# Optimization experiments

Measured on AMD Instinct MI355X. Metric: run time of the kernel, lower is better.

Reference implementation:

```python
import jax, jax.numpy as jnp
import numpy as np
from jax.scipy.linalg import cho_solve

N = 4096        # num nodes
D = 256         # in_dim == out_dim
NUM_HOPS = 2
R = 32          # subspace_dim
ETA = 0.5
EPS_SUB = 0.5   # eps in coeff = r / (n * eps^2)
LN_EPS = 1e-5


def setup_inputs() -> dict:
    rng = np.random.default_rng(0)
    K = NUM_HOPS + 1
    # sparse-ish binary adjacency mask with self loops
    mask = (rng.random((N, N)) < 0.002).astype(np.float32)
    mask = np.maximum(mask, np.eye(N, dtype=np.float32))
    deg = mask.sum(axis=1, keepdims=True)
    A = (mask / deg).astype(np.float32)          # row-stochastic propagation
    L = (np.eye(N, dtype=np.float32) - A)        # normalized Laplacian
    H = rng.standard_normal((N, D)).astype(np.float32)
    # orthonormal subspace bases per hop, as in __init__ (QR of randn)
    U = np.stack([np.linalg.qr(rng.standard_normal((D, R)))[0][:, :R] for _ in range(K)]).astype(np.float32)
    lambda_laps = np.full((K,), 0.1, dtype=np.float32)
    hop_weights = np.full((K,), 1.0 / K, dtype=np.float32)
    threshold = np.full((D,), 0.05, dtype=np.float32)
    gamma = np.ones((D,), dtype=np.float32)
    beta = np.zeros((D,), dtype=np.float32)
    return {
        "H": jnp.asarray(H), "A": jnp.asarray(A), "adj_mask": jnp.asarray(mask),
        "L": jnp.asarray(L), "U": jnp.asarray(U),
        "lambda_laps": jnp.asarray(lambda_laps), "hop_weights": jnp.asarray(hop_weights),
        "threshold": jnp.asarray(threshold), "gamma": jnp.asarray(gamma), "beta": jnp.asarray(beta),
    }


def reference(H, A, adj_mask, L, U, lambda_laps, hop_weights, threshold, gamma, beta):
    n, d = H.shape
    r = U.shape[-1]
    # multi-hop propagation
    hops = [H]
    Hk = H
    for _ in range(NUM_HOPS):
        Hk = A @ Hk
        hops.append(Hk)
    w = jax.nn.softmax(hop_weights)
    laps = jax.nn.softplus(lambda_laps)
    coeff = r / (n * EPS_SUB ** 2)
    neg = (1.0 - adj_mask) * -1e9
    I_r = jnp.eye(r, dtype=H.dtype)
    agg = jnp.zeros_like(H)        # accumulates grad_k.T, shape [n, d]
    lap_total = jnp.zeros_like(H)
    for k, H_k in enumerate(hops):
        Uk = U[k]                  # [d, r]
        Zk = Uk.T @ H_k.T          # [r, n]
        M = I_r + coeff * (Zk @ Zk.T)              # [r, r], SPD
        Lc = jnp.linalg.cholesky(M)
        M_inv = cho_solve((Lc, True), I_r)         # cholesky_inverse
        MZ = M_inv @ Zk                            # [r, n]
        scores = Zk.T @ MZ + neg                   # [n, n] masked subspace attention
        alpha = jax.nn.softmax(scores, axis=1)
        grad_k = (Uk @ (MZ @ alpha.T)).T           # [n, d]
        agg = agg + w[k] * grad_k
        lap_total = lap_total + laps[k] * (L @ H_k)
    H_half = H + ETA * agg - ETA * lap_total
    # soft-threshold (proj is None since in_dim == out_dim)
    H_out = jnp.sign(H_half) * jax.nn.relu(jnp.abs(H_half) - threshold[None, :])
    H_out = H_out + H              # residual
    mu = H_out.mean(axis=-1, keepdims=True)
    var = H_out.var(axis=-1, keepdims=True)
    H_out = (H_out - mu) / jnp.sqrt(var + LN_EPS) * gamma + beta
    # orthogonality loss over all (k, l) pairs
    K = U.shape[0]
    orth_loss = jnp.asarray(0.0, dtype=H.dtype)
    for k in range(K):
        for l in range(k, K):
            G = U[k].T @ U[l]
            orth_loss = orth_loss + jnp.sum(((G - I_r) if l == k else G) ** 2)
    lap_smooth = jnp.sum(H_out * (L @ H_out))  # trace(H^T L H)
    return H_out, orth_loss, lap_smooth, jax.lax.stop_gradient(w)
```

## Files before the change

kernel.cpp:

```cpp
#include <hip/hip_runtime.h>
#include <math.h>

#define NN 4096
#define DD 256
#define KK 3
#define RR 32
#define MAXNNZ 128

static constexpr float ETA    = 0.5f;
static constexpr float COEFF  = 0.03125f;
static constexpr float LN_EPSF = 1e-5f;

#define OFF_H1   0
#define OFF_H2   (NN*DD)
#define OFF_H3   (2*NN*DD)
#define OFF_Y    (3*NN*DD)
#define OFF_P    (OFF_Y + KK*NN*RR)
#define OFF_M    (OFF_P + KK*NN*RR)
#define OFF_MINV (OFF_M + KK*RR*RR)
#define OFF_SCAL (OFF_MINV + KK*RR*RR)
#define OFF_NNZ  (OFF_SCAL + 8)
#define OFF_COLS (OFF_NNZ + NN)
#define OFF_VALS (OFF_COLS + NN*MAXNNZ)
#define OFF_PART (OFF_VALS + NN*MAXNNZ)
#define OFF_ORTH (OFF_PART + NN/4)
#define OFF_W    (OFF_ORTH + 8)

__global__ __launch_bounds__(256, 4)
void k_csr_prep(const float* __restrict__ A, int* __restrict__ nnz,
                int* __restrict__ cols, float* __restrict__ vals,
                const float* __restrict__ hw, const float* __restrict__ ll,
                const float* __restrict__ U,
                float* __restrict__ ws, float* __restrict__ out,
                const float* __restrict__ H) {
  int b = blockIdx.x;
  int t = threadIdx.x;
  if (b >= NN/2) {
    int p = b - NN/2;
    if (p == 6) {
      if (t == 0) {
        float m = fmaxf(fmaxf(hw[0], hw[1]), hw[2]);
        float e0 = expf(hw[0]-m), e1 = expf(hw[1]-m), e2 = expf(hw[2]-m);
        float s = e0 + e1 + e2;
        float w0 = e0/s, w1 = e1/s, w2 = e2/s;
        ws[OFF_SCAL+0] = w0; ws[OFF_SCAL+1] = w1; ws[OFF_SCAL+2] = w2;
        for (int k = 0; k < KK; ++k) {
          float x = ll[k];
          ws[OFF_SCAL+3+k] = (x > 20.f) ? x : log1pf(expf(x));
        }
        out[NN*DD + 2] = w0; out[NN*DD + 3] = w1; out[NN*DD + 4] = w2;
      }
      for (int idx = t; idx < KK*RR*RR; idx += 256) {
        int rr2 = idx % (RR*RR);
        ws[OFF_M + idx] = ((rr2 / RR) == (rr2 % RR)) ? 1.f : 0.f;
      }
      return;
    }
    int k = (p < 3) ? 0 : ((p < 5) ? 1 : 2);
    int l = (p < 3) ? p : ((p < 5) ? p - 2 : 2);
    int a0 = t >> 5, bb = t & 31;
    float s0 = 0.f, s1 = 0.f, s2 = 0.f, s3 = 0.f;
    for (int dd = 0; dd < DD; ++dd) {
      float ul = U[(size_t)l*DD*RR + dd*RR + bb];
      const float* uk = U + (size_t)k*DD*RR + dd*RR;
      s0 += uk[a0]      * ul;
      s1 += uk[a0 + 8]  * ul;
      s2 += uk[a0 + 16] * ul;
      s3 += uk[a0 + 24] * ul;
    }
    if (k == l && bb == a0)      s0 -= 1.f;
    if (k == l && bb == a0 + 8)  s1 -= 1.f;
    if (k == l && bb == a0 + 16) s2 -= 1.f;
    if (k == l && bb == a0 + 24) s3 -= 1.f;
    float sq = s0*s0 + s1*s1 + s2*s2 + s3*s3;
    #pragma unroll
    for (int o = 32; o > 0; o >>= 1) sq += __shfl_xor(sq, o, 64);
    __shared__ float red[4];
    if ((t & 63) == 0) red[t >> 6] = sq;
    __syncthreads();
    if (t == 0) ws[OFF_ORTH + p] = red[0] + red[1] + red[2] + red[3];
    return;
  }
  int w = t >> 6, lane = t & 63;
  int r = w >> 1, h2 = w & 1;
  int i = b * 2 + r;
  __shared__ int   cbuf[2][2][MAXNNZ];
  __shared__ float vbuf[2][2][MAXNNZ];
  __shared__ int   csr_c[2][MAXNNZ];
  __shared__ float csr_v[2][MAXNNZ];
  __shared__ int   cnts[4];
  __shared__ int   nnzs[2];
  __shared__ float Hs[2][2][DD];
  __shared__ float Hs2[2][2][2][DD];
  const float4* row4 = (const float4*)(A + (size_t)i * NN);
  float4 vv[8];
  #pragma unroll
  for (int it = 0; it < 8; ++it) vv[it] = row4[h2*512 + it*64 + lane];
  unsigned long long lower = lane ? (~0ull >> (64 - lane)) : 0ull;
  int base = 0;
  #pragma unroll
  for (int it = 0; it < 8; ++it) {
    float4 v = vv[it];
    int jb = (h2*512 + it*64 + lane) * 4;
    unsigned long long mx = __ballot(v.x != 0.f);
    unsigned long long my = __ballot(v.y != 0.f);
    unsigned long long mz = __ballot(v.z != 0.f);
    unsigned long long mw = __ballot(v.w != 0.f);
    int before = __popcll(mx & lower) + __popcll(my & lower)
               + __popcll(mz & lower) + __popcll(mw & lower);
    int p0 = base + before;
    int bx = (mx >> lane) & 1, by = (my >> lane) & 1, bz = (mz >> lane) & 1;
    if (v.x != 0.f && p0 < MAXNNZ)  { cbuf[r][h2][p0] = jb;   vbuf[r][h2][p0] = v.x; }
    int p1 = p0 + bx;
    if (v.y != 0.f && p1 < MAXNNZ)  { cbuf[r][h2][p1] = jb+1; vbuf[r][h2][p1] = v.y; }
    int p2 = p1 + by;
    if (v.z != 0.f && p2 < MAXNNZ)  { cbuf[r][h2][p2] = jb+2; vbuf[r][h2][p2] = v.z; }
    int p3 = p2 + bz;
    if (v.w != 0.f && p3 < MAXNNZ)  { cbuf[r][h2][p3] = jb+3; vbuf[r][h2][p3] = v.w; }
    base += __popcll(mx) + __popcll(my) + __popcll(mz) + __popcll(mw);
  }
  if (lane == 0) cnts[w] = base < MAXNNZ ? base : MAXNNZ;
  __syncthreads();
  {
    int rr = t >> 7, e0 = t & 127;
    int ii = b * 2 + rr;
    int n0 = cnts[rr*2], n1 = cnts[rr*2 + 1];
    int n = n0 + n1; if (n > MAXNNZ) n = MAXNNZ;
    int npad = (n + 7) & ~7;
    for (int e = e0; e < npad; e += 128) {
      int c; float v;
      if (e < n) {
        if (e < n0) { c = cbuf[rr][0][e];      v = vbuf[rr][0][e]; }
        else        { c = cbuf[rr][1][e - n0]; v = vbuf[rr][1][e - n0]; }
      } else { c = ii; v = 0.f; }
      cols[ii*MAXNNZ + e] = c;
      vals[ii*MAXNNZ + e] = v;
      csr_c[rr][e] = c;
      csr_v[rr][e] = v;
    }
    if (e0 == 0) { nnz[ii] = n; nnzs[rr] = n; }
  }
  __syncthreads();
  {
    int rI = w >> 1, hf = w & 1;
    int row = b * 2 + rI;
    int d4 = lane * 4;
    int n2 = nnzs[rI], npad2 = (n2 + 7) & ~7;
    float4 acc = {0.f, 0.f, 0.f, 0.f};
    float4 own = {0.f, 0.f, 0.f, 0.f};
    for (int e0i = hf*8; e0i < npad2; e0i += 16) {
      int4 c0 = *(const int4*)&csr_c[rI][e0i];
      int4 c1 = *(const int4*)&csr_c[rI][e0i + 4];
      float4 v0 = *(const float4*)&csr_v[rI][e0i];
      float4 v1 = *(const float4*)&csr_v[rI][e0i + 4];
      float4 x0 = *(const float4*)(H + (size_t)c0.x*DD + d4);
      float4 x1 = *(const float4*)(H + (size_t)c0.y*DD + d4);
      float4 x2 = *(const float4*)(H + (size_t)c0.z*DD + d4);
      float4 x3 = *(const float4*)(H + (size_t)c0.w*DD + d4);
      float4 x4 = *(const float4*)(H + (size_t)c1.x*DD + d4);
      float4 x5 = *(const float4*)(H + (size_t)c1.y*DD + d4);
      float4 x6 = *(const float4*)(H + (size_t)c1.z*DD + d4);
      float4 x7 = *(const float4*)(H + (size_t)c1.w*DD + d4);
      if (c0.x == row) own = x0;
      if (c0.y == row) own = x1;
      if (c0.z == row) own = x2;
      if (c0.w == row) own = x3;
      if (c1.x == row) own = x4;
      if (c1.y == row) own = x5;
      if (c1.z == row) own = x6;
      if (c1.w == row) own = x7;
      acc.x += v0.x*x0.x + v0.y*x1.x + v0.z*x2.x + v0.w*x3.x + v1.x*x4.x + v1.y*x5.x + v1.z*x6.x + v1.w*x7.x;
      acc.y += v0.x*x0.y + v0.y*x1.y + v0.z*x2.y + v0.w*x3.y + v1.x*x4.y + v1.y*x5.y + v1.z*x6.y + v1.w*x7.y;
      acc.z += v0.x*x0.z + v0.y*x1.z + v0.z*x2.z + v0.w*x3.z + v1.x*x4.z + v1.y*x5.z + v1.z*x6.z + v1.w*x7.z;
      acc.w += v0.x*x0.w + v0.y*x1.w + v0.z*x2.w + v0.w*x3.w + v1.x*x4.w + v1.y*x5.w + v1.z*x6.w + v1.w*x7.w;
    }
    *(float4*)&Hs2[rI][0][hf][d4] = own;
    *(float4*)&Hs2[rI][1][hf][d4] = acc;
  }
  __syncthreads();
  float* H1 = ws + OFF_H1;
  for (int idx = t; idx < 2*2*DD; idx += 256) {
    int rI2 = idx >> 9, j = (idx >> 8) & 1, d = idx & 255;
    float v2 = Hs2[rI2][j][0][d] + Hs2[rI2][j][1][d];
    Hs[rI2][j][d] = v2;
    if (j == 1) H1[(size_t)(b*2 + rI2)*DD + d] = v2;
  }
  __syncthreads();
  {
    int rI = w >> 1;
    int row = b * 2 + rI;
    int useAcc = w & 1;
    const float* Up = U + (size_t)useAcc*DD*RR;
    float* Yp = ws + OFF_Y + (size_t)useAcc*NN*RR;
    int c = lane & 31, h = lane >> 5;
    float part = 0.f;
    #pragma unroll 8
    for (int d = h*128; d < h*128 + 128; ++d) part += Hs[rI][useAcc][d] * Up[d*RR + c];
    part += __shfl_xor(part, 32, 64);
    if (h == 0) Yp[(size_t)row*RR + c] = part;
  }
}

__device__ __forceinline__ void spmv_quad(const float* __restrict__ X, int row, int lane,
                                          const int* __restrict__ nnz,
                                          const int* __restrict__ cols,
                                          const float* __restrict__ vals,
                                          float4& acc, float4& own) {
  int d4 = lane * 4;
  int n = nnz[row];
  int npad = (n + 7) & ~7;
  const int* ci = cols + row*MAXNNZ;
  const float* vi = vals + row*MAXNNZ;
  for (int e0 = 0; e0 < npad; e0 += 8) {
    int4 c0 = *(const int4*)(ci + e0);
    int4 c1 = *(const int4*)(ci + e0 + 4);
    float4 v0 = *(const float4*)(vi + e0);
    float4 v1 = *(const float4*)(vi + e0 + 4);
    float4 x0 = *(const float4*)(X + (size_t)c0.x*DD + d4);
    float4 x1 = *(const float4*)(X + (size_t)c0.y*DD + d4);
    float4 x2 = *(const float4*)(X + (size_t)c0.z*DD + d4);
    float4 x3 = *(const float4*)(X + (size_t)c0.w*DD + d4);
    float4 x4 = *(const float4*)(X + (size_t)c1.x*DD + d4);
    float4 x5 = *(const float4*)(X + (size_t)c1.y*DD + d4);
    float4 x6 = *(const float4*)(X + (size_t)c1.z*DD + d4);
    float4 x7 = *(const float4*)(X + (size_t)c1.w*DD + d4);
    if (c0.x == row) own = x0;
    if (c0.y == row) own = x1;
    if (c0.z == row) own = x2;
    if (c0.w == row) own = x3;
    if (c1.x == row) own = x4;
    if (c1.y == row) own = x5;
    if (c1.z == row) own = x6;
    if (c1.w == row) own = x7;
    acc.x += v0.x*x0.x + v0.y*x1.x + v0.z*x2.x + v0.w*x3.x + v1.x*x4.x + v1.y*x5.x + v1.z*x6.x + v1.w*x7.x;
    acc.y += v0.x*x0.y + v0.y*x1.y + v0.z*x2.y + v0.w*x3.y + v1.x*x4.y + v1.y*x5.y + v1.z*x6.y + v1.w*x7.y;
    acc.z += v0.x*x0.z + v0.y*x1.z + v0.z*x2.z + v0.w*x3.z + v1.x*x4.z + v1.y*x5.z + v1.z*x6.z + v1.w*x7.z;
    acc.w += v0.x*x0.w + v0.y*x1.w + v0.z*x2.w + v0.w*x3.w + v1.x*x4.w + v1.y*x5.w + v1.z*x6.w + v1.w*x7.w;
  }
}

__global__ void k_spmvy(const float* __restrict__ X, float* __restrict__ Hout,
                        const int* __restrict__ nnz, const int* __restrict__ cols,
                        const float* __restrict__ vals,
                        const float* __restrict__ Uo, float* __restrict__ Yo,
                        const float* __restrict__ Un, float* __restrict__ Yn,
                        const float* __restrict__ Yg, float* __restrict__ Mg) {
  int t = threadIdx.x;
  if (blockIdx.x >= NN/4) {
    if (!Yg) return;
    int gb = blockIdx.x - NN/4;
    int k = gb >> 5, g = gb & 31;
    __shared__ float Ys[128*RR];
    const float* Yk = Yg + (size_t)k*NN*RR + (size_t)g*128*RR;
    for (int idx = t; idx < 128*RR; idx += 256) Ys[idx] = Yk[idx];
    __syncthreads();
    int a = t >> 3, b4 = (t & 7) * 4;
    float s0 = 0.f, s1 = 0.f, s2 = 0.f, s3 = 0.f;
    for (int i = 0; i < 128; ++i) {
      float ya = Ys[i*RR + a];
      s0 += ya * Ys[i*RR + b4];
      s1 += ya * Ys[i*RR + b4 + 1];
      s2 += ya * Ys[i*RR + b4 + 2];
      s3 += ya * Ys[i*RR + b4 + 3];
    }
    atomicAdd(&Mg[k*RR*RR + a*RR + b4],     COEFF * s0);
    atomicAdd(&Mg[k*RR*RR + a*RR + b4 + 1], COEFF * s1);
    atomicAdd(&Mg[k*RR*RR + a*RR + b4 + 2], COEFF * s2);
    atomicAdd(&Mg[k*RR*RR + a*RR + b4 + 3], COEFF * s3);
    return;
  }
  int r = t >> 6, lane = t & 63;
  int row = blockIdx.x * 4 + r;
  int d4 = lane * 4;
  float4 acc = {0.f, 0.f, 0.f, 0.f};
  float4 own = {0.f, 0.f, 0.f, 0.f};
  spmv_quad(X, row, lane, nnz, cols, vals, acc, own);
  *(float4*)(Hout + (size_t)row*DD + d4) = acc;
  if (!Uo && !Un) return;
  __shared__ float Hs[4][2][DD];
  *(float4*)&Hs[r][0][d4] = own;
  *(float4*)&Hs[r][1][d4] = acc;
  __syncthreads();
  int c = lane & 31, h = lane >> 5;
  if (Uo) {
    float part = 0.f;
    #pragma unroll 8
    for (int d = h*128; d < h*128 + 128; ++d) part += Hs[r][0][d] * Uo[d*RR + c];
    part += __shfl_xor(part, 32, 64);
    if (h == 0) Yo[(size_t)row*RR + c] = part;
  }
  if (Un) {
    float part = 0.f;
    #pragma unroll 8
    for (int d = h*128; d < h*128 + 128; ++d) part += Hs[r][1][d] * Un[d*RR + c];
    part += __shfl_xor(part, 32, 64);
    if (h == 0) Yn[(size_t)row*RR + c] = part;
  }
}

__global__ __launch_bounds__(1024) void k_gram(const float* __restrict__ Yk, float* __restrict__ Mk) {
  __shared__ float Ys[128*RR];
  int t = threadIdx.x;
  const float* Yb = Yk + (size_t)blockIdx.x*128*RR;
  for (int idx = t; idx < 128*RR; idx += 1024) Ys[idx] = Yb[idx];
  __syncthreads();
  int a = t >> 5, b = t & 31;
  float s = 0.f;
  for (int i = 0; i < 128; ++i) s += Ys[i*RR + a] * Ys[i*RR + b];
  atomicAdd(&Mk[a*RR + b], COEFF * s);
}

__global__ __launch_bounds__(256) void k_gj(const float* __restrict__ M, float* __restrict__ Minv,
                                            const float* __restrict__ U, float* __restrict__ W) {
  int k = blockIdx.x;
  int g = blockIdx.y;
  int t = threadIdx.x;
  __shared__ float B[RR][2*RR + 1];
  for (int idx = t; idx < RR*2*RR; idx += 256) {
    int r = idx >> 6, c = idx & 63;
    B[r][c] = (c < RR) ? M[k*RR*RR + r*RR + c] : ((c - RR == r) ? 1.f : 0.f);
  }
  __syncthreads();
  if (t < 64) {
    for (int p = 0; p < RR; ++p) {
      float rd = 1.f / B[p][p];
      float pb = B[p][t] * rd;
      float f[RR];
      #pragma unroll
      for (int r = 0; r < RR; ++r) f[r] = B[r][p];
      B[p][t] = pb;
      #pragma unroll
      for (int r = 0; r < RR; ++r) {
        if (r == p) continue;
        B[r][t] -= f[r] * pb;
      }
    }
  }
  __syncthreads();
  if (g == 0)
    for (int idx = t; idx < RR*RR; idx += 256)
      Minv[k*RR*RR + idx] = B[idx >> 5][RR + (idx & 31)];
  for (int e = 0; e < 8; ++e) {
    int idx = t + e*256;
    int d = g*64 + (idx >> 5), rr2 = idx & 31;
    const float* ud = U + (size_t)k*DD*RR + (size_t)d*RR;
    float s = 0.f;
    #pragma unroll
    for (int a = 0; a < RR; ++a) s += ud[a] * B[a][RR + rr2];
    W[(size_t)k*DD*RR + (size_t)d*RR + rr2] = s;
  }
}

__global__ __launch_bounds__(256) void k_attn(const float* __restrict__ Y, const float* __restrict__ Minv,
                       float* __restrict__ P, const int* __restrict__ nnz,
                       const int* __restrict__ cols, const float* __restrict__ vals,
                       const float* __restrict__ H2, float* __restrict__ H3) {
  int k = blockIdx.y;
  int t = threadIdx.x;
  int w = t >> 6, lane = t & 63;
  if (blockIdx.x >= NN/4) {
    if (k != 0) return;
    int row = (blockIdx.x - NN/4) * 4 + w;
    float4 acc = {0.f, 0.f, 0.f, 0.f};
    float4 own;
    spmv_quad(H2, row, lane, nnz, cols, vals, acc, own);
    *(float4*)(H3 + (size_t)row*DD + lane*4) = acc;
    return;
  }
  int i = blockIdx.x * 4 + w;
  const float* Yk = Y + (size_t)k*NN*RR;
  __shared__ float Mi[RR*RR];
  __shared__ float Yi[4][RR];
  __shared__ float qv[4][RR];
  __shared__ float sc[4][MAXNNZ];
  __shared__ float Yc[4][32][RR + 1];
  for (int idx = t; idx < RR*RR; idx += 256) Mi[idx] = Minv[k*RR*RR + idx];
  if (lane < RR) Yi[w][lane] = Yk[(size_t)i*RR + lane];
  sc[w][lane] = -1e30f; sc[w][lane+64] = -1e30f;
  __syncthreads();
  if (lane < RR) {
    float s = 0.f;
    #pragma unroll 8
    for (int a = 0; a < RR; ++a) s += Mi[a*RR + lane] * Yi[w][a];
    qv[w][lane] = s;
  }
  int g = lane >> 2, a4 = lane & 3;
  const float* qq = &qv[w][8*a4];
  float q0 = qq[0], q1 = qq[1], q2 = qq[2], q3 = qq[3];
  float q4 = qq[4], q5 = qq[5], q6 = qq[6], q7 = qq[7];
  int n = nnz[i], npad = (n + 7) & ~7;
  const int* ci = cols + i*MAXNNZ;
  for (int e0 = 0; e0 < npad; e0 += 16) {
    int e = e0 + g;
    int ee = (e < npad) ? e : 0;
    int col = ci[ee];
    const float4* yr = (const float4*)(Yk + (size_t)col*RR + 8*a4);
    float4 y0 = yr[0], y1 = yr[1];
    if (e < 32) {
      *(float4*)&Yc[w][e][8*a4]     = y0;
      *(float4*)&Yc[w][e][8*a4 + 4] = y1;
    }
    float s = y0.x*q0 + y0.y*q1 + y0.z*q2 + y0.w*q3
            + y1.x*q4 + y1.y*q5 + y1.z*q6 + y1.w*q7;
    s += __shfl_xor(s, 1, 64);
    s += __shfl_xor(s, 2, 64);
    if (a4 == 0 && e < npad) sc[w][e] = (e < n) ? s : -1e30f;
  }
  float s0 = sc[w][lane], s1 = sc[w][lane+64];
  float m = fmaxf(s0, s1);
  #pragma unroll
  for (int o = 32; o > 0; o >>= 1) m = fmaxf(m, __shfl_xor(m, o, 64));
  float e0v = expf(s0 - m), e1v = expf(s1 - m);
  sc[w][lane] = e0v; sc[w][lane+64] = e1v;
  float l = e0v + e1v;
  #pragma unroll
  for (int o = 32; o > 0; o >>= 1) l += __shfl_xor(l, o, 64);
  float linv = 1.f / l;
  int c = lane & 31, h = lane >> 5;
  float acc = 0.f;
  int lim = npad < 32 ? npad : 32;
  for (int e = h; e < lim; e += 2) acc += sc[w][e] * Yc[w][e][c];
  for (int e = 32 + h; e < npad; e += 2) acc += sc[w][e] * Yk[(size_t)ci[e]*RR + c];
  acc += __shfl_xor(acc, 32, 64);
  if (lane < RR) P[(size_t)k*NN*RR + (size_t)i*RR + lane] = acc * linv;
}

__global__ void k_epi(const float* __restrict__ H0, const float* __restrict__ ws,
                      const float* __restrict__ thr,
                      const float* __restrict__ gma, const float* __restrict__ bta,
                      float* __restrict__ out) {
  __shared__ float Us[DD][RR+1];
  __shared__ float Ps[8][KK*RR];
  int t = threadIdx.x;
  int ty = t >> 5, tx = t & 31;
  int row0 = blockIdx.x * 8;
  const float* P    = ws + OFF_P;
  const float* scal = ws + OFF_SCAL;
  const float* W    = ws + OFF_W;
  for (int idx = t; idx < 8*KK*RR; idx += 256) {
    int rl = idx / (KK*RR), kr = idx % (KK*RR);
    int k = kr / RR, rr2 = kr % RR;
    Ps[rl][kr] = P[(size_t)k*NN*RR + (size_t)(row0+rl)*RR + rr2];
  }
  float lp0 = scal[3], lp1 = scal[4], lp2 = scal[5];
  float gacc[8];
  #pragma unroll
  for (int j = 0; j < 8; ++j) gacc[j] = 0.f;
  for (int k = 0; k < KK; ++k) {
    __syncthreads();
    for (int idx = t; idx < DD*RR/4; idx += 256) {
      float4 w4 = *(const float4*)(W + (size_t)k*DD*RR + (size_t)idx*4);
      int d = (idx*4) >> 5, c = (idx*4) & 31;
      Us[d][c] = w4.x; Us[d][c+1] = w4.y; Us[d][c+2] = w4.z; Us[d][c+3] = w4.w;
    }
    __syncthreads();
    float wk = scal[k];
    #pragma unroll
    for (int j = 0; j < 8; ++j) {
      int d = tx + 32*j;
      float s = 0.f;
      #pragma unroll
      for (int rr2 = 0; rr2 < RR; ++rr2) s += Ps[ty][k*RR + rr2] * Us[d][rr2];
      gacc[j] += wk * s;
    }
  }
  int i = row0 + ty;
  const float* H1 = ws + OFF_H1;
  const float* H2 = ws + OFF_H2;
  const float* H3 = ws + OFF_H3;
  float v[8]; float sum = 0.f, sumsq = 0.f;
  #pragma unroll
  for (int j = 0; j < 8; ++j) {
    int d = tx + 32*j;
    size_t idx = (size_t)i*DD + d;
    float h0 = H0[idx], h1 = H1[idx], h2 = H2[idx], h3 = H3[idx];
    float lap = lp0*(h0-h1) + lp1*(h1-h2) + lp2*(h2-h3);
    float hf = h0 + ETA*gacc[j] - ETA*lap;
    float a = fabsf(hf) - thr[d];
    float sft = (a > 0.f) ? copysignf(a, hf) : 0.f;
    float x = sft + h0;
    v[j] = x; sum += x; sumsq += x*x;
  }
  #pragma unroll
  for (int o = 16; o > 0; o >>= 1) {
    sum   += __shfl_xor(sum, o, 32);
    sumsq += __shfl_xor(sumsq, o, 32);
  }
  float mu  = sum * (1.f/DD);
  float var = sumsq * (1.f/DD) - mu*mu;
  float inv = rsqrtf(var + LN_EPSF);
  #pragma unroll
  for (int j = 0; j < 8; ++j) {
    int d = tx + 32*j;
    out[(size_t)i*DD + d] = (v[j] - mu) * inv * gma[d] + bta[d];
  }
}

__global__ void k_lapsm(const float* __restrict__ Hout, const int* __restrict__ nnz,
                        const int* __restrict__ cols, const float* __restrict__ vals,
                        float* __restrict__ partial) {
  int t = threadIdx.x;
  int row = blockIdx.x * 4 + (t >> 6);
  int d4 = (t & 63) * 4;
  int n = nnz[row];
  int npad = (n + 7) & ~7;
  const int* ci = cols + row*MAXNNZ;
  const float* vi = vals + row*MAXNNZ;
  float4 acc = {0.f, 0.f, 0.f, 0.f};
  for (int e0 = 0; e0 < npad; e0 += 8) {
    int4 c0 = *(const int4*)(ci + e0);
    int4 c1 = *(const int4*)(ci + e0 + 4);
    float4 v0 = *(const float4*)(vi + e0);
    float4 v1 = *(const float4*)(vi + e0 + 4);
    float4 x0 = *(const float4*)(Hout + (size_t)c0.x*DD + d4);
    float4 x1 = *(const float4*)(Hout + (size_t)c0.y*DD + d4);
    float4 x2 = *(const float4*)(Hout + (size_t)c0.z*DD + d4);
    float4 x3 = *(const float4*)(Hout + (size_t)c0.w*DD + d4);
    float4 x4 = *(const float4*)(Hout + (size_t)c1.x*DD + d4);
    float4 x5 = *(const float4*)(Hout + (size_t)c1.y*DD + d4);
    float4 x6 = *(const float4*)(Hout + (size_t)c1.z*DD + d4);
    float4 x7 = *(const float4*)(Hout + (size_t)c1.w*DD + d4);
    acc.x += v0.x*x0.x + v0.y*x1.x + v0.z*x2.x + v0.w*x3.x + v1.x*x4.x + v1.y*x5.x + v1.z*x6.x + v1.w*x7.x;
    acc.y += v0.x*x0.y + v0.y*x1.y + v0.z*x2.y + v0.w*x3.y + v1.x*x4.y + v1.y*x5.y + v1.z*x6.y + v1.w*x7.y;
    acc.z += v0.x*x0.z + v0.y*x1.z + v0.z*x2.z + v0.w*x3.z + v1.x*x4.z + v1.y*x5.z + v1.z*x6.z + v1.w*x7.z;
    acc.w += v0.x*x0.w + v0.y*x1.w + v0.z*x2.w + v0.w*x3.w + v1.x*x4.w + v1.y*x5.w + v1.z*x6.w + v1.w*x7.w;
  }
  float4 h = *(const float4*)(Hout + (size_t)row*DD + d4);
  float part = h.x*(h.x-acc.x) + h.y*(h.y-acc.y) + h.z*(h.z-acc.z) + h.w*(h.w-acc.w);
  #pragma unroll
  for (int o = 32; o > 0; o >>= 1) part += __shfl_xor(part, o, 64);
  __shared__ float red[4];
  if ((t & 63) == 0) red[t >> 6] = part;
  __syncthreads();
  if (t == 0) partial[blockIdx.x] = red[0] + red[1] + red[2] + red[3];
}

__global__ void k_red(const float* __restrict__ ws, float* __restrict__ out) {
  const float* partial = ws + OFF_PART;
  int t = threadIdx.x;
  float4 p = *(const float4*)(partial + t*4);
  float s = p.x + p.y + p.z + p.w;
  #pragma unroll
  for (int o = 32; o > 0; o >>= 1) s += __shfl_xor(s, o, 64);
  __shared__ float red[4];
  if ((t & 63) == 0) red[t >> 6] = s;
  __syncthreads();
  if (t == 0) {
    out[1] = red[0] + red[1] + red[2] + red[3];
    const float* op = ws + OFF_ORTH;
    out[0] = op[0] + op[1] + op[2] + op[3] + op[4] + op[5];
  }
}

extern "C" void kernel_launch(void* const* d_in, const int* in_sizes, int n_in,
                              void* d_out, int out_size, void* d_ws, size_t ws_size,
                              hipStream_t stream) {
  const float* H   = (const float*)d_in[0];
  const float* A   = (const float*)d_in[1];
  const float* U   = (const float*)d_in[4];
  const float* ll  = (const float*)d_in[5];
  const float* hw  = (const float*)d_in[6];
  const float* thr = (const float*)d_in[7];
  const float* gma = (const float*)d_in[8];
  const float* bta = (const float*)d_in[9];
  float* out = (float*)d_out;
  float* ws  = (float*)d_ws;
  int* nnz   = (int*)(ws + OFF_NNZ);
  int* cols  = (int*)(ws + OFF_COLS);
  float* vals = ws + OFF_VALS;
  float* Y = ws + OFF_Y;

  k_csr_prep<<<NN/2 + 7, 256, 0, stream>>>(A, nnz, cols, vals, hw, ll, U, ws, out, H);
  k_spmvy<<<NN/4 + 64, 256, 0, stream>>>(ws + OFF_H1, ws + OFF_H2, nnz, cols, vals,
                                         nullptr, nullptr, U + (size_t)2*DD*RR, Y + (size_t)2*NN*RR,
                                         Y, ws + OFF_M);
  k_gram<<<NN/128, 1024, 0, stream>>>(Y + (size_t)2*NN*RR, ws + OFF_M + 2*RR*RR);
  dim3 ggj(KK, 4);
  k_gj<<<ggj, 256, 0, stream>>>(ws + OFF_M, ws + OFF_MINV, U, ws + OFF_W);
  dim3 gattn(NN/4 + NN/4, KK);
  k_attn<<<gattn, 256, 0, stream>>>(Y, ws + OFF_MINV, ws + OFF_P, nnz, cols, vals,
                                    ws + OFF_H2, ws + OFF_H3);
  k_epi<<<NN/8, 256, 0, stream>>>(H, ws, thr, gma, bta, out);
  k_lapsm<<<NN/4, 256, 0, stream>>>(out, nnz, cols, vals, ws + OFF_PART);
  k_red<<<1, 256, 0, stream>>>(ws, out + NN*DD);
}
```

Before: 281.3 us.

## Move H3 SpMV into gram kernel and simplify first-hop SpMV reduction

The third-hop SpMV blocks move out of the attention kernel and into the Gram-matrix kernel, which now runs 256-thread blocks that each compute four outputs and issue fewer atomics. This removes the wasted blocks in k_attn for k!=0 and overlaps the SpMV with the small Gram reduction. In the CSR prep kernel, one wave now does the whole first-hop SpMV per row instead of splitting it across two waves. That drops a shared-memory reduction and a barrier, but halves parallelism in that phase.

```diff
diff --git a/kernel.cpp b/kernel.cpp
--- a/kernel.cpp
+++ b/kernel.cpp
@@ -91,7 +91,6 @@
   __shared__ int   cnts[4];
   __shared__ int   nnzs[2];
   __shared__ float Hs[2][2][DD];
-  __shared__ float Hs2[2][2][2][DD];
   const float4* row4 = (const float4*)(A + (size_t)i * NN);
   float4 vv[8];
   #pragma unroll
@@ -141,14 +140,15 @@
     if (e0 == 0) { nnz[ii] = n; nnzs[rr] = n; }
   }
   __syncthreads();
-  {
-    int rI = w >> 1, hf = w & 1;
+  float* H1 = ws + OFF_H1;
+  if ((w & 1) == 0) {
+    int rI = w >> 1;
     int row = b * 2 + rI;
     int d4 = lane * 4;
     int n2 = nnzs[rI], npad2 = (n2 + 7) & ~7;
     float4 acc = {0.f, 0.f, 0.f, 0.f};
     float4 own = {0.f, 0.f, 0.f, 0.f};
-    for (int e0i = hf*8; e0i < npad2; e0i += 16) {
+    for (int e0i = 0; e0i < npad2; e0i += 8) {
       int4 c0 = *(const int4*)&csr_c[rI][e0i];
       int4 c1 = *(const int4*)&csr_c[rI][e0i + 4];
       float4 v0 = *(const float4*)&csr_v[rI][e0i];
@@ -174,16 +174,9 @@
       acc.z += v0.x*x0.z + v0.y*x1.z + v0.z*x2.z + v0.w*x3.z + v1.x*x4.z + v1.y*x5.z + v1.z*x6.z + v1.w*x7.z;
       acc.w += v0.x*x0.w + v0.y*x1.w + v0.z*x2.w + v0.w*x3.w + v1.x*x4.w + v1.y*x5.w + v1.z*x6.w + v1.w*x7.w;
     }
-    *(float4*)&Hs2[rI][0][hf][d4] = own;
-    *(float4*)&Hs2[rI][1][hf][d4] = acc;
-  }
-  __syncthreads();
-  float* H1 = ws + OFF_H1;
-  for (int idx = t; idx < 2*2*DD; idx += 256) {
-    int rI2 = idx >> 9, j = (idx >> 8) & 1, d = idx & 255;
-    float v2 = Hs2[rI2][j][0][d] + Hs2[rI2][j][1][d];
-    Hs[rI2][j][d] = v2;
-    if (j == 1) H1[(size_t)(b*2 + rI2)*DD + d] = v2;
+    *(float4*)(H1 + (size_t)row*DD + d4) = acc;
+    *(float4*)&Hs[rI][0][d4] = own;
+    *(float4*)&Hs[rI][1][d4] = acc;
   }
   __syncthreads();
   {
@@ -298,16 +291,37 @@
   }
 }
 
-__global__ __launch_bounds__(1024) void k_gram(const float* __restrict__ Yk, float* __restrict__ Mk) {
-  __shared__ float Ys[128*RR];
-  int t = threadIdx.x;
-  const float* Yb = Yk + (size_t)blockIdx.x*128*RR;
-  for (int idx = t; idx < 128*RR; idx += 1024) Ys[idx] = Yb[idx];
-  __syncthreads();
-  int a = t >> 5, b = t & 31;
-  float s = 0.f;
-  for (int i = 0; i < 128; ++i) s += Ys[i*RR + a] * Ys[i*RR + b];
-  atomicAdd(&Mk[a*RR + b], COEFF * s);
+__global__ __launch_bounds__(256) void k_gram2h3(const float* __restrict__ Yk2, float* __restrict__ Mk2,
+                                                 const int* __restrict__ nnz, const int* __restrict__ cols,
+                                                 const float* __restrict__ vals,
+                                                 const float* __restrict__ H2, float* __restrict__ H3) {
+  int t = threadIdx.x;
+  if (blockIdx.x < 32) {
+    __shared__ float Ys[128*RR];
+    const float* Yb = Yk2 + (size_t)blockIdx.x*128*RR;
+    for (int idx = t; idx < 128*RR; idx += 256) Ys[idx] = Yb[idx];
+    __syncthreads();
+    int a = t >> 3, b4 = (t & 7) * 4;
+    float s0 = 0.f, s1 = 0.f, s2 = 0.f, s3 = 0.f;
+    for (int i = 0; i < 128; ++i) {
+      float ya = Ys[i*RR + a];
+      s0 += ya * Ys[i*RR + b4];
+      s1 += ya * Ys[i*RR + b4 + 1];
+      s2 += ya * Ys[i*RR + b4 + 2];
+      s3 += ya * Ys[i*RR + b4 + 3];
+    }
+    atomicAdd(&Mk2[a*RR + b4],     COEFF * s0);
+    atomicAdd(&Mk2[a*RR + b4 + 1], COEFF * s1);
+    atomicAdd(&Mk2[a*RR + b4 + 2], COEFF * s2);
+    atomicAdd(&Mk2[a*RR + b4 + 3], COEFF * s3);
+    return;
+  }
+  int w = t >> 6, lane = t & 63;
+  int row = (blockIdx.x - 32) * 4 + w;
+  float4 acc = {0.f, 0.f, 0.f, 0.f};
+  float4 own;
+  spmv_quad(H2, row, lane, nnz, cols, vals, acc, own);
+  *(float4*)(H3 + (size_t)row*DD + lane*4) = acc;
 }
 
 __global__ __launch_bounds__(256) void k_gj(const float* __restrict__ M, float* __restrict__ Minv,
@@ -353,20 +367,10 @@
 
 __global__ __launch_bounds__(256) void k_attn(const float* __restrict__ Y, const float* __restrict__ Minv,
                        float* __restrict__ P, const int* __restrict__ nnz,
-                       const int* __restrict__ cols, const float* __restrict__ vals,
-                       const float* __restrict__ H2, float* __restrict__ H3) {
+                       const int* __restrict__ cols) {
   int k = blockIdx.y;
   int t = threadIdx.x;
   int w = t >> 6, lane = t & 63;
-  if (blockIdx.x >= NN/4) {
-    if (k != 0) return;
-    int row = (blockIdx.x - NN/4) * 4 + w;
-    float4 acc = {0.f, 0.f, 0.f, 0.f};
-    float4 own;
-    spmv_quad(H2, row, lane, nnz, cols, vals, acc, own);
-    *(float4*)(H3 + (size_t)row*DD + lane*4) = acc;
-    return;
-  }
   int i = blockIdx.x * 4 + w;
   const float* Yk = Y + (size_t)k*NN*RR;
   __shared__ float Mi[RR*RR];
@@ -574,12 +578,12 @@
   k_spmvy<<<NN/4 + 64, 256, 0, stream>>>(ws + OFF_H1, ws + OFF_H2, nnz, cols, vals,
                                          nullptr, nullptr, U + (size_t)2*DD*RR, Y + (size_t)2*NN*RR,
                                          Y, ws + OFF_M);
-  k_gram<<<NN/128, 1024, 0, stream>>>(Y + (size_t)2*NN*RR, ws + OFF_M + 2*RR*RR);
+  k_gram2h3<<<32 + NN/4, 256, 0, stream>>>(Y + (size_t)2*NN*RR, ws + OFF_M + 2*RR*RR,
+                                           nnz, cols, vals, ws + OFF_H2, ws + OFF_H3);
   dim3 ggj(KK, 4);
   k_gj<<<ggj, 256, 0, stream>>>(ws + OFF_M, ws + OFF_MINV, U, ws + OFF_W);
-  dim3 gattn(NN/4 + NN/4, KK);
-  k_attn<<<gattn, 256, 0, stream>>>(Y, ws + OFF_MINV, ws + OFF_P, nnz, cols, vals,
-                                    ws + OFF_H2, ws + OFF_H3);
+  dim3 gattn(NN/4, KK);
+  k_attn<<<gattn, 256, 0, stream>>>(Y, ws + OFF_MINV, ws + OFF_P, nnz, cols);
   k_epi<<<NN/8, 256, 0, stream>>>(H, ws, thr, gma, bta, out);
   k_lapsm<<<NN/4, 256, 0, stream>>>(out, nnz, cols, vals, ws + OFF_PART);
   k_red<<<1, 256, 0, stream>>>(ws, out + NN*DD);
```

Result: no change. 284.8 us (+1.2%).
